# Kernel tuning notes

Measured on AMD Instinct MI355X. Metric: run time of the kernel, lower is better.

Reference implementation:

```python
import jax, jax.numpy as jnp
import numpy as np

BLOCK = 128
LN_EPS = 1e-5


def _dequant_linear(x, w, s):
    # w: [out, in], s: [out//128, in//128] block scales -> y = x @ (w * expand(s)).T
    ws = w * jnp.repeat(jnp.repeat(s, BLOCK, axis=0), BLOCK, axis=1)
    return x @ ws.T


def setup_inputs() -> dict:
    H, L, M, S, N = 2048, 8192, 4096, 1024, 8192
    key = jax.random.key(0)
    ks = jax.random.split(key, 12)
    sc = 0.02  # weight init scale to keep activations sane
    return {
        "x": jax.random.normal(ks[0], (N, H), dtype=jnp.float32),
        "w_qkv": jax.random.normal(ks[1], (L, H), dtype=jnp.float32) * sc,
        "s_qkv": jnp.ones((L // BLOCK, H // BLOCK), dtype=jnp.float32),
        "w_z": jax.random.normal(ks[2], (M, H), dtype=jnp.float32) * sc,
        "s_z": jnp.ones((M // BLOCK, H // BLOCK), dtype=jnp.float32),
        "w_b": jax.random.normal(ks[3], (S, H), dtype=jnp.float32) * sc,
        "s_b": jnp.ones((S // BLOCK, H // BLOCK), dtype=jnp.float32),
        "w_a": jax.random.normal(ks[4], (S, H), dtype=jnp.float32) * sc,
        "s_a": jnp.ones((S // BLOCK, H // BLOCK), dtype=jnp.float32),
        "d_qkv": jax.random.normal(ks[5], (H, L), dtype=jnp.float32) * sc,
        "d_z": jax.random.normal(ks[6], (H, M), dtype=jnp.float32) * sc,
        "d_b": jax.random.normal(ks[7], (H, S), dtype=jnp.float32) * sc,
        "d_a": jax.random.normal(ks[8], (H, S), dtype=jnp.float32) * sc,
        "gamma": jnp.ones((H,), dtype=jnp.float32),
        "beta": jnp.zeros((H,), dtype=jnp.float32),
    }


def reference(x, w_qkv, s_qkv, w_z, s_z, w_b, s_b, w_a, s_a,
              d_qkv, d_z, d_b, d_a, gamma, beta):
    qkv = _dequant_linear(x, w_qkv, s_qkv) @ d_qkv.T
    z = _dequant_linear(x, w_z, s_z) @ d_z.T
    b = _dequant_linear(x, w_b, s_b) @ d_b.T
    a = _dequant_linear(x, w_a, s_a) @ d_a.T
    h = qkv + z + b + a
    mu = jnp.mean(h, axis=-1, keepdims=True)
    var = jnp.mean(jnp.square(h - mu), axis=-1, keepdims=True)
    return (h - mu) * jax.lax.rsqrt(var + LN_EPS) * gamma + beta
```

## Files before the change

kernel.cpp:

```cpp
#include <hip/hip_runtime.h>
#include <hip/hip_bf16.h>
#include <stdint.h>


typedef unsigned short u16;
typedef __bf16 bf16x8 __attribute__((ext_vector_type(8)));
typedef float f32x4 __attribute__((ext_vector_type(4)));

#define H 2048
#define KTOT 14336

__device__ __forceinline__ u16 f2b(float f) {
    union { float f; uint32_t u; } v; v.f = f;
    uint32_t u = v.u;
    return (u16)((u + 0x7fffu + ((u >> 16) & 1u)) >> 16);
}

__device__ __forceinline__ void gld16(const u16* g, u16* l) {
    __builtin_amdgcn_global_load_lds((__attribute__((address_space(1))) void*)g,
                                     (__attribute__((address_space(3))) void*)l,
                                     16, 0, 0);
}

__global__ __launch_bounds__(256) void prep_pack(const float* __restrict__ dq,
                                                 const float* __restrict__ dz,
                                                 const float* __restrict__ db,
                                                 const float* __restrict__ da,
                                                 const float* __restrict__ x,
                                                 u16* __restrict__ Acat,
                                                 u16* __restrict__ Xb) {
    int bid = blockIdx.x;
    if (bid >= 28672) {
        size_t i = (((size_t)(bid - 28672)) * 256 + threadIdx.x) * 8;
        float4 a = *(const float4*)(x + i);
        float4 b = *(const float4*)(x + i + 4);
        uint32_t p0 = (uint32_t)f2b(a.x) | ((uint32_t)f2b(a.y) << 16);
        uint32_t p1 = (uint32_t)f2b(a.z) | ((uint32_t)f2b(a.w) << 16);
        uint32_t p2 = (uint32_t)f2b(b.x) | ((uint32_t)f2b(b.y) << 16);
        uint32_t p3 = (uint32_t)f2b(b.z) | ((uint32_t)f2b(b.w) << 16);
        *(uint4*)(Xb + i) = make_uint4(p0, p1, p2, p3);
        return;
    }
    const float* src; int kshift, kmask, coloff, base;
    if (bid < 16384)      { src = dq; kshift = 13; kmask = 8191; coloff = 0;     base = 0; }
    else if (bid < 24576) { src = dz; kshift = 12; kmask = 4095; coloff = 8192;  base = 16384; }
    else if (bid < 26624) { src = db; kshift = 10; kmask = 1023; coloff = 12288; base = 24576; }
    else                  { src = da; kshift = 10; kmask = 1023; coloff = 13312; base = 26624; }
    size_t idx = ((size_t)(bid - base) * 256 + threadIdx.x) * 4;
    int r = (int)(idx >> kshift);
    int c = (int)(idx & (size_t)kmask);
    float4 v = *(const float4*)(src + idx);
    ushort4 o = make_ushort4(f2b(v.x), f2b(v.y), f2b(v.z), f2b(v.w));
    *(ushort4*)(Acat + (size_t)r * KTOT + coloff + c) = o;
}

__global__ __launch_bounds__(256) void prep_w(const float* __restrict__ wq, const float* __restrict__ sq,
                                              const float* __restrict__ wz, const float* __restrict__ sz,
                                              const float* __restrict__ wb, const float* __restrict__ sb,
                                              const float* __restrict__ wa, const float* __restrict__ sa,
                                              u16* __restrict__ dst) {
    __shared__ float tile[64][65];
    int by = blockIdx.y;
    const float* w; const float* s; int coloff, ybase;
    if (by < 128)      { w = wq; s = sq; coloff = 0;     ybase = 0; }
    else if (by < 192) { w = wz; s = sz; coloff = 8192;  ybase = 128; }
    else if (by < 208) { w = wb; s = sb; coloff = 12288; ybase = 192; }
    else               { w = wa; s = sa; coloff = 13312; ybase = 208; }
    const int t = threadIdx.x;
    const int i0 = blockIdx.x * 64, k0 = (by - ybase) * 64;
    const int c4 = (t & 15) * 4;
    const int r0 = t >> 4;
    const int sib = i0 >> 7;
#pragma unroll
    for (int rr = 0; rr < 4; ++rr) {
        int r = r0 + rr * 16;
        float sc = s[((k0 + r) >> 7) * (H / 128) + sib];
        float4 v = *(const float4*)(w + (size_t)(k0 + r) * H + i0 + c4);
        tile[r][c4 + 0] = v.x * sc;
        tile[r][c4 + 1] = v.y * sc;
        tile[r][c4 + 2] = v.z * sc;
        tile[r][c4 + 3] = v.w * sc;
    }
    __syncthreads();
#pragma unroll
    for (int rr = 0; rr < 4; ++rr) {
        int i = r0 + rr * 16;
        ushort4 o = make_ushort4(f2b(tile[c4 + 0][i]), f2b(tile[c4 + 1][i]),
                                 f2b(tile[c4 + 2][i]), f2b(tile[c4 + 3][i]));
        *(ushort4*)(dst + (size_t)(i0 + i) * KTOT + coloff + k0 + c4) = o;
    }
}

__global__ __launch_bounds__(256) void reduce4_cvt(const float* __restrict__ P,
                                                   u16* __restrict__ G) {
    size_t i = ((size_t)blockIdx.x * 256 + threadIdx.x) * 4;
    const size_t st = (size_t)H * H;
    float4 a = *(const float4*)(P + i);
    float4 b = *(const float4*)(P + i + st);
    float4 c = *(const float4*)(P + i + 2 * st);
    float4 d = *(const float4*)(P + i + 3 * st);
    ushort4 o = make_ushort4(f2b(a.x + b.x + c.x + d.x),
                             f2b(a.y + b.y + c.y + d.y),
                             f2b(a.z + b.z + c.z + d.z),
                             f2b(a.w + b.w + c.w + d.w));
    *(ushort4*)(G + i) = o;
}

__device__ __forceinline__ void gemm256_core(const u16* __restrict__ A,
                                             const u16* __restrict__ B,
                                             float* __restrict__ C,
                                             int lda, int ldb, int N, int klen) {
    __shared__ __align__(16) u16 As[32768];
    __shared__ __align__(16) u16 Bs[32768];
    const int t = threadIdx.x;
    const int lane = t & 63;
    const int wave = t >> 6;
    const int wm = (wave >> 2) * 128;
    const int wn = (wave & 3) * 64;
    const size_t bm0 = (size_t)blockIdx.y * 256;
    const size_t bn0 = (size_t)blockIdx.x * 256;
    const int kstart = blockIdx.z * klen;
    const int NS = klen >> 5;

    const int srow = t >> 2;
    const int scol = ((t & 3) ^ ((t >> 3) & 3)) * 8;
    const u16* ga = A + (bm0 + srow) * (size_t)lda + kstart + scol;
    const u16* gb = B + (bn0 + srow) * (size_t)ldb + kstart + scol;
    const size_t lda128 = (size_t)128 * lda;
    const size_t ldb128 = (size_t)128 * ldb;
    u16* const lwa = As + (t & ~63) * 8;
    u16* const lwb = Bs + (t & ~63) * 8;

    const int lr = lane & 15;
    const int fro = (((lane >> 4) ^ ((lr >> 1) & 3))) * 8;
    const u16* const fra = As + (wm + lr) * 32 + fro;
    const u16* const frb = Bs + (wn + lr) * 32 + fro;

    f32x4 acc[8][4] = {};

    auto STAGE = [&](int sidx) {
        const int sl = (sidx & 3) * 8192;
        const u16* a = ga + (size_t)sidx * 32;
        const u16* b = gb + (size_t)sidx * 32;
        gld16(a,          lwa + sl);
        gld16(a + lda128, lwa + sl + 4096);
        gld16(b,          lwb + sl);
        gld16(b + ldb128, lwb + sl + 4096);
    };
    auto COMPUTE = [&](int sidx) {
        const int sl = (sidx & 3) * 8192;
        const u16* fa = fra + sl;
        const u16* fb = frb + sl;
        bf16x8 af[8], bfr[4];
#pragma unroll
        for (int i = 0; i < 8; ++i) af[i] = *(const bf16x8*)(fa + i * 512);
#pragma unroll
        for (int j = 0; j < 4; ++j) bfr[j] = *(const bf16x8*)(fb + j * 512);
        __builtin_amdgcn_s_setprio(1);
#pragma unroll
        for (int mi = 0; mi < 8; ++mi)
#pragma unroll
            for (int ni = 0; ni < 4; ++ni)
                acc[mi][ni] = __builtin_amdgcn_mfma_f32_16x16x32_bf16(af[mi], bfr[ni], acc[mi][ni], 0, 0, 0);
        __builtin_amdgcn_s_setprio(0);
    };

    STAGE(0); STAGE(1); STAGE(2);
    int s = 0;
    for (; s < NS - 3; ++s) {
        STAGE(s + 3);
        asm volatile("s_waitcnt vmcnt(12)" ::: "memory");
        __builtin_amdgcn_s_barrier();
        COMPUTE(s);
        __builtin_amdgcn_s_barrier();
    }
    asm volatile("s_waitcnt vmcnt(8)" ::: "memory");
    __builtin_amdgcn_s_barrier();
    COMPUTE(s); ++s;
    __builtin_amdgcn_s_barrier();
    asm volatile("s_waitcnt vmcnt(4)" ::: "memory");
    __builtin_amdgcn_s_barrier();
    COMPUTE(s); ++s;
    __builtin_amdgcn_s_barrier();
    asm volatile("s_waitcnt vmcnt(0)" ::: "memory");
    __builtin_amdgcn_s_barrier();
    COMPUTE(s);

    const int en = (int)bn0 + wn + lr;
    const int em = (int)bm0 + wm + (lane >> 4) * 4;
#pragma unroll
    for (int mi = 0; mi < 8; ++mi)
#pragma unroll
        for (int ni = 0; ni < 4; ++ni)
#pragma unroll
            for (int r = 0; r < 4; ++r)
                C[(size_t)(em + mi * 16 + r) * N + (en + ni * 16)] = acc[mi][ni][r];
}

__global__ __launch_bounds__(512, 2) void gemm_kb_part(const u16* __restrict__ A,
                                                       const u16* __restrict__ B,
                                                       float* __restrict__ C,
                                                       int lda, int ldb, int N, int klen) {
    gemm256_core(A, B, C + (size_t)blockIdx.z * H * H, lda, ldb, N, klen);
}

__global__ __launch_bounds__(512, 2) void gemm_kc_store(const u16* __restrict__ A,
                                                        const u16* __restrict__ B,
                                                        float* __restrict__ C,
                                                        int lda, int ldb, int N, int klen) {
    gemm256_core(A, B, C, lda, ldb, N, klen);
}

__global__ __launch_bounds__(256) void layernorm_kernel(float* __restrict__ h,
                                                        const float* __restrict__ gamma,
                                                        const float* __restrict__ beta) {
    const int t = threadIdx.x;
    float* row = h + (size_t)blockIdx.x * H;
    float4 v0 = ((const float4*)row)[t];
    float4 v1 = ((const float4*)row)[t + 256];
    float s = v0.x + v0.y + v0.z + v0.w + v1.x + v1.y + v1.z + v1.w;
    float q = v0.x * v0.x + v0.y * v0.y + v0.z * v0.z + v0.w * v0.w +
              v1.x * v1.x + v1.y * v1.y + v1.z * v1.z + v1.w * v1.w;
#pragma unroll
    for (int off = 32; off > 0; off >>= 1) {
        s += __shfl_down(s, off, 64);
        q += __shfl_down(q, off, 64);
    }
    __shared__ float sw[4], sq[4];
    if ((t & 63) == 0) { sw[t >> 6] = s; sq[t >> 6] = q; }
    __syncthreads();
    s = sw[0] + sw[1] + sw[2] + sw[3];
    q = sq[0] + sq[1] + sq[2] + sq[3];
    float mu = s * (1.0f / H);
    float var = q * (1.0f / H) - mu * mu;
    float rs = rsqrtf(var + 1e-5f);
    float4 g0 = ((const float4*)gamma)[t], g1 = ((const float4*)gamma)[t + 256];
    float4 b0 = ((const float4*)beta)[t],  b1 = ((const float4*)beta)[t + 256];
    v0.x = (v0.x - mu) * rs * g0.x + b0.x;
    v0.y = (v0.y - mu) * rs * g0.y + b0.y;
    v0.z = (v0.z - mu) * rs * g0.z + b0.z;
    v0.w = (v0.w - mu) * rs * g0.w + b0.w;
    v1.x = (v1.x - mu) * rs * g1.x + b1.x;
    v1.y = (v1.y - mu) * rs * g1.y + b1.y;
    v1.z = (v1.z - mu) * rs * g1.z + b1.z;
    v1.w = (v1.w - mu) * rs * g1.w + b1.w;
    ((float4*)row)[t] = v0;
    ((float4*)row)[t + 256] = v1;
}

extern "C" void kernel_launch(void* const* d_in, const int* in_sizes, int n_in,
                              void* d_out, int out_size, void* d_ws, size_t ws_size,
                              hipStream_t stream) {
    const float* x     = (const float*)d_in[0];
    const float* w_qkv = (const float*)d_in[1];
    const float* s_qkv = (const float*)d_in[2];
    const float* w_z   = (const float*)d_in[3];
    const float* s_z   = (const float*)d_in[4];
    const float* w_b   = (const float*)d_in[5];
    const float* s_b   = (const float*)d_in[6];
    const float* w_a   = (const float*)d_in[7];
    const float* s_a   = (const float*)d_in[8];
    const float* dq    = (const float*)d_in[9];
    const float* dz    = (const float*)d_in[10];
    const float* db    = (const float*)d_in[11];
    const float* da    = (const float*)d_in[12];
    const float* gamma = (const float*)d_in[13];
    const float* beta  = (const float*)d_in[14];
    float* out = (float*)d_out;

    uint8_t* ws = (uint8_t*)d_ws;
    u16* Acat = (u16*)(ws);
    u16* Bcat = (u16*)(ws + 58720256);
    u16* Xb   = (u16*)(ws + 117440512);
    u16* G    = (u16*)(ws + 150994944);

    prep_pack<<<36864, 256, 0, stream>>>(dq, dz, db, da, x, Acat, Xb);
    prep_w<<<dim3(32, 224), 256, 0, stream>>>(w_qkv, s_qkv, w_z, s_z,
                                              w_b, s_b, w_a, s_a, Bcat);
    gemm_kb_part<<<dim3(8, 8, 4), 512, 0, stream>>>(Acat, Bcat, out, KTOT, KTOT, H, 3584);
    reduce4_cvt<<<4096, 256, 0, stream>>>(out, G);
    gemm_kc_store<<<dim3(8, 32, 1), 512, 0, stream>>>(Xb, G, out, H, H, H, H);
    layernorm_kernel<<<8192, 256, 0, stream>>>(out, gamma, beta);
}
```

Measured before the change: 589.2 us.

## Rework GEMM core into double-buffered K=64 tiles with quadrant-interleaved loads

Replaces the 4-stage K=32 LDS ring in the shared 256x256 GEMM core with a 2-buffer K=64 pipeline. Each tile is split into four quadrant MFMA phases, with global-to-LDS loads for the next tile interleaved between them and a new XOR swizzle for 64-wide rows. It also flattens the grid to 1D with a block-index remap that spreads work across XCDs/L2, and passes tile offsets explicitly. The change targets load latency hiding and cache locality, at the cost of more barriers per tile and a more intricate vmcnt schedule.

New measurement: 537.8 us. 8.7% less time.

```diff
diff --git a/kernel.cpp b/kernel.cpp
--- a/kernel.cpp
+++ b/kernel.cpp
@@ -109,106 +109,141 @@
 __device__ __forceinline__ void gemm256_core(const u16* __restrict__ A,
                                              const u16* __restrict__ B,
                                              float* __restrict__ C,
-                                             int lda, int ldb, int N, int klen) {
-    __shared__ __align__(16) u16 As[32768];
-    __shared__ __align__(16) u16 Bs[32768];
+                                             int lda, int ldb, int N, int klen,
+                                             int bm0, int bn0, int kstart) {
+    __shared__ __align__(16) u16 As[2][16384];
+    __shared__ __align__(16) u16 Bs[2][16384];
     const int t = threadIdx.x;
     const int lane = t & 63;
     const int wave = t >> 6;
     const int wm = (wave >> 2) * 128;
     const int wn = (wave & 3) * 64;
-    const size_t bm0 = (size_t)blockIdx.y * 256;
-    const size_t bn0 = (size_t)blockIdx.x * 256;
-    const int kstart = blockIdx.z * klen;
-    const int NS = klen >> 5;
-
-    const int srow = t >> 2;
-    const int scol = ((t & 3) ^ ((t >> 3) & 3)) * 8;
-    const u16* ga = A + (bm0 + srow) * (size_t)lda + kstart + scol;
-    const u16* gb = B + (bn0 + srow) * (size_t)ldb + kstart + scol;
-    const size_t lda128 = (size_t)128 * lda;
-    const size_t ldb128 = (size_t)128 * ldb;
-    u16* const lwa = As + (t & ~63) * 8;
-    u16* const lwb = Bs + (t & ~63) * 8;
+    const int NT = klen >> 6;
+
+    const int srow = t >> 3;
+    const int sc = ((t & 7) ^ ((t >> 3) & 7)) * 8;
+    const u16* gA = A + (size_t)(bm0 + srow) * lda + kstart + sc;
+    const u16* gB = B + (size_t)(bn0 + srow) * ldb + kstart + sc;
+    const size_t a64 = (size_t)64 * lda, b64 = (size_t)64 * ldb;
+    u16* const lA = (u16*)As + (t & ~63) * 8;
+    u16* const lB = (u16*)Bs + (t & ~63) * 8;
 
     const int lr = lane & 15;
-    const int fro = (((lane >> 4) ^ ((lr >> 1) & 3))) * 8;
-    const u16* const fra = As + (wm + lr) * 32 + fro;
-    const u16* const frb = Bs + (wn + lr) * 32 + fro;
-
-    f32x4 acc[8][4] = {};
-
-    auto STAGE = [&](int sidx) {
-        const int sl = (sidx & 3) * 8192;
-        const u16* a = ga + (size_t)sidx * 32;
-        const u16* b = gb + (size_t)sidx * 32;
-        gld16(a,          lwa + sl);
-        gld16(a + lda128, lwa + sl + 4096);
-        gld16(b,          lwb + sl);
-        gld16(b + ldb128, lwb + sl + 4096);
+    const int ch0 = (((lane >> 4)    ) ^ (lane & 7)) * 8;
+    const int ch1 = (((lane >> 4) | 4) ^ (lane & 7)) * 8;
+
+    f32x4 a00[4][2] = {}, a01[4][2] = {}, a10[4][2] = {}, a11[4][2] = {};
+    bf16x8 aF[4][2], b0F[2][2], b1F[2][2];
+
+    auto RD_A = [&](const u16* buf, int qm) {
+#pragma unroll
+        for (int f = 0; f < 4; ++f) {
+            const u16* p = buf + (wm + qm * 64 + f * 16 + lr) * 64;
+            aF[f][0] = *(const bf16x8*)(p + ch0);
+            aF[f][1] = *(const bf16x8*)(p + ch1);
+        }
     };
-    auto COMPUTE = [&](int sidx) {
-        const int sl = (sidx & 3) * 8192;
-        const u16* fa = fra + sl;
-        const u16* fb = frb + sl;
-        bf16x8 af[8], bfr[4];
-#pragma unroll
-        for (int i = 0; i < 8; ++i) af[i] = *(const bf16x8*)(fa + i * 512);
-#pragma unroll
-        for (int j = 0; j < 4; ++j) bfr[j] = *(const bf16x8*)(fb + j * 512);
+    auto RD_B = [&](const u16* buf, int qn) {
+#pragma unroll
+        for (int g = 0; g < 2; ++g) {
+            const u16* p = buf + (wn + qn * 32 + g * 16 + lr) * 64;
+            if (qn == 0) { b0F[g][0] = *(const bf16x8*)(p + ch0);
+                           b0F[g][1] = *(const bf16x8*)(p + ch1); }
+            else         { b1F[g][0] = *(const bf16x8*)(p + ch0);
+                           b1F[g][1] = *(const bf16x8*)(p + ch1); }
+        }
+    };
+    auto MM = [&](int qm, int qn) {
         __builtin_amdgcn_s_setprio(1);
 #pragma unroll
-        for (int mi = 0; mi < 8; ++mi)
-#pragma unroll
-            for (int ni = 0; ni < 4; ++ni)
-                acc[mi][ni] = __builtin_amdgcn_mfma_f32_16x16x32_bf16(af[mi], bfr[ni], acc[mi][ni], 0, 0, 0);
+        for (int f = 0; f < 4; ++f)
+#pragma unroll
+            for (int g = 0; g < 2; ++g) {
+                f32x4& d = (qm == 0) ? (qn == 0 ? a00[f][g] : a01[f][g])
+                                     : (qn == 0 ? a10[f][g] : a11[f][g]);
+                const bf16x8* bb = (qn == 0) ? b0F[g] : b1F[g];
+                d = __builtin_amdgcn_mfma_f32_16x16x32_bf16(aF[f][0], bb[0], d, 0, 0, 0);
+                d = __builtin_amdgcn_mfma_f32_16x16x32_bf16(aF[f][1], bb[1], d, 0, 0, 0);
+            }
         __builtin_amdgcn_s_setprio(0);
     };
-
-    STAGE(0); STAGE(1); STAGE(2);
-    int s = 0;
-    for (; s < NS - 3; ++s) {
-        STAGE(s + 3);
-        asm volatile("s_waitcnt vmcnt(12)" ::: "memory");
-        __builtin_amdgcn_s_barrier();
-        COMPUTE(s);
-        __builtin_amdgcn_s_barrier();
-    }
-    asm volatile("s_waitcnt vmcnt(8)" ::: "memory");
+    auto STG = [&](int wbuf, int rnd, int kt) {
+        if (rnd < 4)
+            gld16(gB + (size_t)rnd * b64 + kt, lB + wbuf * 16384 + rnd * 4096);
+        else {
+            const int rb = (rnd == 4) ? 0 : (rnd == 5) ? 2 : (rnd == 6) ? 1 : 3;
+            gld16(gA + (size_t)rb * a64 + kt, lA + wbuf * 16384 + rb * 4096);
+        }
+    };
+
+#pragma unroll
+    for (int r = 0; r < 8; ++r) STG(0, r, 0);
+    asm volatile("s_waitcnt vmcnt(2)" ::: "memory");
     __builtin_amdgcn_s_barrier();
-    COMPUTE(s); ++s;
-    __builtin_amdgcn_s_barrier();
-    asm volatile("s_waitcnt vmcnt(4)" ::: "memory");
-    __builtin_amdgcn_s_barrier();
-    COMPUTE(s); ++s;
-    __builtin_amdgcn_s_barrier();
-    asm volatile("s_waitcnt vmcnt(0)" ::: "memory");
-    __builtin_amdgcn_s_barrier();
-    COMPUTE(s);
-
-    const int en = (int)bn0 + wn + lr;
-    const int em = (int)bm0 + wm + (lane >> 4) * 4;
-#pragma unroll
-    for (int mi = 0; mi < 8; ++mi)
-#pragma unroll
-        for (int ni = 0; ni < 4; ++ni)
-#pragma unroll
-            for (int r = 0; r < 4; ++r)
-                C[(size_t)(em + mi * 16 + r) * N + (en + ni * 16)] = acc[mi][ni][r];
+    asm volatile("" ::: "memory");
+
+    for (int tt = 0; tt < NT; ++tt) {
+        const u16* Ar = (const u16*)As + (tt & 1) * 16384;
+        const u16* Br = (const u16*)Bs + (tt & 1) * 16384;
+        const int wbuf = (tt + 1) & 1;
+        const int ktn = (tt + 1) * 64;
+        const bool st = (tt + 1) < NT;
+        RD_A(Ar, 0); RD_B(Br, 0);
+        if (st) { STG(wbuf, 0, ktn); STG(wbuf, 1, ktn); }
+        __builtin_amdgcn_s_barrier(); asm volatile("" ::: "memory");
+        MM(0, 0);
+        __builtin_amdgcn_s_barrier(); asm volatile("" ::: "memory");
+        RD_B(Br, 1);
+        if (st) { STG(wbuf, 2, ktn); STG(wbuf, 3, ktn);
+                  asm volatile("s_waitcnt vmcnt(4)" ::: "memory"); }
+        else    { asm volatile("s_waitcnt vmcnt(0)" ::: "memory"); }
+        __builtin_amdgcn_s_barrier(); asm volatile("" ::: "memory");
+        MM(0, 1);
+        __builtin_amdgcn_s_barrier(); asm volatile("" ::: "memory");
+        RD_A(Ar, 1);
+        if (st) { STG(wbuf, 4, ktn); STG(wbuf, 5, ktn); }
+        __builtin_amdgcn_s_barrier(); asm volatile("" ::: "memory");
+        MM(1, 1);
+        __builtin_amdgcn_s_barrier(); asm volatile("" ::: "memory");
+        if (st) { STG(wbuf, 6, ktn); STG(wbuf, 7, ktn);
+                  asm volatile("s_waitcnt vmcnt(2)" ::: "memory"); }
+        __builtin_amdgcn_s_barrier(); asm volatile("" ::: "memory");
+        MM(1, 0);
+        __builtin_amdgcn_s_barrier(); asm volatile("" ::: "memory");
+    }
+
+    const int en = bn0 + wn + lr;
+    const int em0 = bm0 + wm + (lane >> 4) * 4;
+#pragma unroll
+    for (int f = 0; f < 4; ++f)
+#pragma unroll
+        for (int g = 0; g < 2; ++g)
+#pragma unroll
+            for (int r = 0; r < 4; ++r) {
+                C[(size_t)(em0 + f * 16 + r) * N + en + g * 16]            = a00[f][g][r];
+                C[(size_t)(em0 + f * 16 + r) * N + en + 32 + g * 16]      = a01[f][g][r];
+                C[(size_t)(em0 + 64 + f * 16 + r) * N + en + g * 16]      = a10[f][g][r];
+                C[(size_t)(em0 + 64 + f * 16 + r) * N + en + 32 + g * 16] = a11[f][g][r];
+            }
 }
 
 __global__ __launch_bounds__(512, 2) void gemm_kb_part(const u16* __restrict__ A,
                                                        const u16* __restrict__ B,
                                                        float* __restrict__ C,
                                                        int lda, int ldb, int N, int klen) {
-    gemm256_core(A, B, C + (size_t)blockIdx.z * H * H, lda, ldb, N, klen);
+    int L = ((blockIdx.x & 7) << 5) + (blockIdx.x >> 3);
+    int bx = L & 7, by = (L >> 3) & 7, bz = L >> 6;
+    gemm256_core(A, B, C + (size_t)bz * H * H, lda, ldb, N, klen,
+                 by * 256, bx * 256, bz * klen);
 }
 
 __global__ __launch_bounds__(512, 2) void gemm_kc_store(const u16* __restrict__ A,
                                                         const u16* __restrict__ B,
                                                         float* __restrict__ C,
                                                         int lda, int ldb, int N, int klen) {
-    gemm256_core(A, B, C, lda, ldb, N, klen);
+    int L = ((blockIdx.x & 7) << 5) + (blockIdx.x >> 3);
+    int bx = L & 7, by = L >> 3;
+    gemm256_core(A, B, C, lda, ldb, N, klen, by * 256, bx * 256, 0);
 }
 
 __global__ __launch_bounds__(256) void layernorm_kernel(float* __restrict__ h,
@@ -277,8 +312,8 @@
     prep_pack<<<36864, 256, 0, stream>>>(dq, dz, db, da, x, Acat, Xb);
     prep_w<<<dim3(32, 224), 256, 0, stream>>>(w_qkv, s_qkv, w_z, s_z,
                                               w_b, s_b, w_a, s_a, Bcat);
-    gemm_kb_part<<<dim3(8, 8, 4), 512, 0, stream>>>(Acat, Bcat, out, KTOT, KTOT, H, 3584);
+    gemm_kb_part<<<256, 512, 0, stream>>>(Acat, Bcat, out, KTOT, KTOT, H, 3584);
     reduce4_cvt<<<4096, 256, 0, stream>>>(out, G);
-    gemm_kc_store<<<dim3(8, 32, 1), 512, 0, stream>>>(Xb, G, out, H, H, H, H);
+    gemm_kc_store<<<256, 512, 0, stream>>>(Xb, G, out, H, H, H, H);
     layernorm_kernel<<<8192, 256, 0, stream>>>(out, gamma, beta);
 }
```
